# Kernel tuning notes

Hardware: AMD Instinct MI355X
Metric: run time of the kernel (lower is better)

Reference implementation:

```python
import jax, jax.numpy as jnp
import numpy as np

N, E, G = 8000, 32000, 256   # nodes, edges, graphs
F, H = 680, 10               # in-features, GAT heads
HF = F * H                   # 6800


def setup_inputs() -> dict:
    key = jax.random.key(0)
    ks = jax.random.split(key, 12)
    s = lambda i, shape, sc: (jax.random.normal(ks[i], shape, jnp.float32) * sc)
    x = jax.random.normal(ks[0], (N, F), jnp.float32)
    edge_index = jax.random.randint(ks[1], (2, E), 0, N)
    batch = jnp.arange(N) // (N // G)   # contiguous, every graph non-empty
    return dict(
        x=x, edge_index=edge_index, batch=batch,
        W_gat=s(2, (F, HF), 0.05), a_src=s(3, (H, F), 0.05), a_dst=s(4, (H, F), 0.05),
        b_gat=jnp.zeros((HF,), jnp.float32),
        W_gcn=s(5, (HF, HF), 0.01), b_gcn=jnp.zeros((HF,), jnp.float32),
        W1=s(6, (2 * HF, 512), 0.02), b1=jnp.zeros((512,), jnp.float32),
        W2=s(7, (512, 128), 0.05), b2=jnp.zeros((128,), jnp.float32),
        W3=s(8, (128, 64), 0.05), b3=jnp.zeros((64,), jnp.float32),
    )


def _self_loops(edge_index):
    loop = jnp.arange(N)
    return (jnp.concatenate([edge_index[0], loop]),
            jnp.concatenate([edge_index[1], loop]))


def _gat(x, src, dst, W, a_s, a_d, b):
    xh = (x @ W).reshape(N, H, F)                          # [N,H,F]
    al_s = jnp.einsum('nhf,hf->nh', xh, a_s)               # src attention logits
    al_d = jnp.einsum('nhf,hf->nh', xh, a_d)
    e = jax.nn.leaky_relu(al_s[src] + al_d[dst], 0.2)      # [Etot,H]
    m = jax.ops.segment_max(e, dst, num_segments=N)        # segment softmax over dst
    ex = jnp.exp(e - m[dst])
    z = jax.ops.segment_sum(ex, dst, num_segments=N)
    alpha = ex / (z[dst] + 1e-16)
    out = jax.ops.segment_sum(alpha[:, :, None] * xh[src], dst, num_segments=N)
    return out.reshape(N, HF) + b                          # concat heads + bias


def _gcn(x, src, dst, W, b):
    deg = jax.ops.segment_sum(jnp.ones_like(dst, jnp.float32), dst, num_segments=N)
    dinv = jax.lax.rsqrt(deg)                              # deg>=1 due to self-loops
    norm = dinv[src] * dinv[dst]
    xw = x @ W
    return jax.ops.segment_sum(norm[:, None] * xw[src], dst, num_segments=N) + b


def reference(x, edge_index, batch, W_gat, a_src, a_dst, b_gat, W_gcn, b_gcn,
              W1, b1, W2, b2, W3, b3):
    src, dst = _self_loops(edge_index)
    h = jax.nn.relu(_gat(x, src, dst, W_gat, a_src, a_dst, b_gat))  # dropout = id (eval)
    h = jax.nn.relu(_gcn(h, src, dst, W_gcn, b_gcn))
    gmp = jax.ops.segment_max(h, batch, num_segments=G)
    cnt = jax.ops.segment_sum(jnp.ones((N,), jnp.float32), batch, num_segments=G)
    gap = jax.ops.segment_sum(h, batch, num_segments=G) / cnt[:, None]
    g = jnp.concatenate([gmp, gap], axis=1)                # [G, 2*HF]
    g = jax.nn.relu(g @ W1 + b1)
    g = g @ W2 + b2
    return g @ W3 + b3                                     # [G, 64]
```

## Files before the change

kernel.cpp:

```cpp
#include <hip/hip_runtime.h>
#include <cstdint>
#include <cstddef>

#define DEVFN static __device__ __forceinline__

typedef __attribute__((ext_vector_type(8))) short short8;
typedef __attribute__((ext_vector_type(4))) float f32x4;

constexpr int NN  = 8000;
constexpr int NE  = 32000;
constexpr int ET  = NE + NN;
constexpr int NG  = 256;
constexpr int F   = 680;
constexpr int NH  = 10;
constexpr int HF  = 6800;

constexpr int MP   = 8192;
constexpr int KP1  = 704;
constexpr int NP   = 6912;
constexpr int KP2  = 6848;
constexpr int KM1P = 13632;

DEVFN unsigned short f2bf(float f) {
  unsigned u = __float_as_uint(f);
  u += 0x7fffu + ((u >> 16) & 1u);
  return (unsigned short)(u >> 16);
}
DEVFN float bf2f(unsigned short b) { return __uint_as_float(((unsigned)b) << 16); }

DEVFN int perm64(int k, int r) {
  return (((k >> 3) ^ (r & 7)) << 3) | (k & 7);
}

DEVFN void gload16(const void* g, void* l) {
  __builtin_amdgcn_global_load_lds(
      (const __attribute__((address_space(1))) unsigned int*)g,
      (__attribute__((address_space(3))) unsigned int*)l, 16, 0, 0);
}

DEVFN f32x4 mfma_16x16x32_bf16(short8 a, short8 b, f32x4 c) {
  asm("v_mfma_f32_16x16x32_bf16 %0, %1, %2, %0" : "+v"(c) : "v"(a), "v"(b));
  return c;
}

template<int OUT_MODE, bool BIAS, bool RELU, bool SWZ>
__global__ __launch_bounds__(512, 2) void gemm256(
    const unsigned short* __restrict__ A, const unsigned short* __restrict__ BT,
    void* __restrict__ C, const float* __restrict__ bias,
    int K, int cstride, int nvalid, int Mt, int KC) {
  __shared__ alignas(16) char Lds[131072];
  const int tid = threadIdx.x;
  const int wave = tid >> 6, lane = tid & 63;
  const int wm = wave >> 2, wn = wave & 3;
  const int g4 = lane >> 4, l15 = lane & 15;
  const int xorc = l15 & 7;
  const int brow = (wn & 1) * 64;

  int bm, bn;
  if (SWZ) {
    const int xcd = blockIdx.x & 7;
    const int j = blockIdx.x >> 3;
    bm = j & 31;
    bn = (j >> 5) * 8 + xcd;
    const int Nt = (nvalid + 255) >> 8;
    if (bn >= Nt) return;
  } else {
    bm = blockIdx.x % Mt;
    bn = blockIdx.x / Mt;
  }

  const int NTt = K >> 6;
  const int kb = blockIdx.z * KC;
  const int NT = min(KC, NTt - kb);
  const unsigned short* Ag = A + (size_t)bm * 256 * K + (size_t)kb * 64;
  const unsigned short* Bg = BT + (size_t)bn * 256 * K + (size_t)kb * 64;

  const int srow = tid >> 3;
  const int schk = (tid & 7) * 8;

  auto stageHalf = [&](const unsigned short* G, int t, int op, int h) {
    char* base = Lds + ((((t & 1) << 2) | (op << 1) | h) << 14) + (wave << 10);
    const unsigned short* src = G + (size_t)(h * 128 + srow) * K + (size_t)t * 64 + schk;
    gload16(src, base);
    gload16(src + (size_t)64 * K, base + 8192);
  };

  const char* Ab0 = Lds + (((0 << 2) | (0 << 1) | wm) << 14);
  const char* Ab1 = Lds + (((1 << 2) | (0 << 1) | wm) << 14);
  const char* Bb0 = Lds + (((0 << 2) | (1 << 1) | (wn >> 1)) << 14);
  const char* Bb1 = Lds + (((1 << 2) | (1 << 1) | (wn >> 1)) << 14);

  f32x4 acc[8][4];
#pragma unroll
  for (int i = 0; i < 8; i++)
#pragma unroll
    for (int j = 0; j < 4; j++) acc[i][j] = (f32x4){0.f, 0.f, 0.f, 0.f};

  short8 aR[4][2], b0[2][2], b1[2][2];

#define READ_A(BASE, QM) do {                                                   \
  _Pragma("unroll") for (int i2 = 0; i2 < 4; ++i2)                              \
  _Pragma("unroll") for (int ks = 0; ks < 2; ++ks)                              \
    aR[i2][ks] = *(const short8*)((BASE) + ((QM) * 64 + i2 * 16 + l15) * 128    \
                                  + ((((ks << 2) | g4) ^ xorc) << 4));          \
} while (0)

#define READ_B(BASE, QN, DST) do {                                              \
  _Pragma("unroll") for (int j2 = 0; j2 < 2; ++j2)                              \
  _Pragma("unroll") for (int ks = 0; ks < 2; ++ks)                              \
    DST[j2][ks] = *(const short8*)((BASE) + (brow + (QN) * 32 + j2 * 16 + l15) * 128 \
                                   + ((((ks << 2) | g4) ^ xorc) << 4));         \
} while (0)

#define MMAQ(QM, QN, BREG) do {                                                 \
  _Pragma("unroll") for (int i2 = 0; i2 < 4; ++i2)                              \
  _Pragma("unroll") for (int j2 = 0; j2 < 2; ++j2)                              \
  _Pragma("unroll") for (int ks = 0; ks < 2; ++ks)                              \
    acc[(QM) * 4 + i2][(QN) * 2 + j2] =                                         \
        mfma_16x16x32_bf16(aR[i2][ks], BREG[j2][ks], acc[(QM) * 4 + i2][(QN) * 2 + j2]); \
} while (0)

  if (NT > 0) {
    stageHalf(Ag, 0, 0, 0); stageHalf(Ag, 0, 0, 1);
    stageHalf(Bg, 0, 1, 0); stageHalf(Bg, 0, 1, 1);
  }
  if (NT > 1) {
    stageHalf(Ag, 1, 0, 0); stageHalf(Ag, 1, 0, 1);
    stageHalf(Bg, 1, 1, 0); stageHalf(Bg, 1, 1, 1);
    asm volatile("s_waitcnt vmcnt(8)" ::: "memory");
  } else {
    asm volatile("s_waitcnt vmcnt(0)" ::: "memory");
  }
  asm volatile("s_barrier" ::: "memory");

  for (int t = 0; t < NT; ++t) {
    const char* Ac = (t & 1) ? Ab1 : Ab0;
    const char* Bc = (t & 1) ? Bb1 : Bb0;
    const bool pf = (t + 2 < NT);

    READ_A(Ac, 0);
    READ_B(Bc, 0, b0);
    __builtin_amdgcn_s_setprio(1);
    MMAQ(0, 0, b0);
    __builtin_amdgcn_s_setprio(0);

    READ_B(Bc, 1, b1);
    __builtin_amdgcn_s_setprio(1);
    MMAQ(0, 1, b1);
    __builtin_amdgcn_s_setprio(0);

    asm volatile("s_barrier" ::: "memory");
    if (pf) { stageHalf(Bg, t + 2, 1, 0); stageHalf(Bg, t + 2, 1, 1); }

    READ_A(Ac, 1);
    __builtin_amdgcn_s_setprio(1);
    MMAQ(1, 1, b1);
    __builtin_amdgcn_s_setprio(0);

    asm volatile("s_barrier" ::: "memory");
    if (pf) { stageHalf(Ag, t + 2, 0, 0); stageHalf(Ag, t + 2, 0, 1); }

    __builtin_amdgcn_s_setprio(1);
    MMAQ(1, 0, b0);
    __builtin_amdgcn_s_setprio(0);

    if (pf) asm volatile("s_waitcnt vmcnt(8)" ::: "memory");
    else    asm volatile("s_waitcnt vmcnt(0)" ::: "memory");
    asm volatile("s_barrier" ::: "memory");
  }

#undef READ_A
#undef READ_B
#undef MMAQ

  const int m0 = bm * 256 + wm * 128;
  const int n0 = bn * 256 + wn * 64;
  const int rb = g4 * 4;
#pragma unroll
  for (int i = 0; i < 8; i++) {
#pragma unroll
    for (int j = 0; j < 4; j++) {
      int c = n0 + j * 16 + l15;
      if (c >= nvalid) continue;
      float bv = BIAS ? bias[c] : 0.f;
#pragma unroll
      for (int tt = 0; tt < 4; tt++) {
        int r = m0 + i * 16 + rb + tt;
        float v = acc[i][j][tt] + bv;
        if (RELU) v = fmaxf(v, 0.f);
        if (OUT_MODE == 0) {
          ((float*)C)[(size_t)r * cstride + c] = v;
        } else if (OUT_MODE == 1) {
          ((unsigned short*)C)[(size_t)r * cstride + c] = f2bf(v);
        } else if (OUT_MODE == 2) {
          int pos = (c & ~63) + perm64(c & 63, r);
          ((unsigned short*)C)[(size_t)r * cstride + pos] = f2bf(v);
        } else {
          ((float*)C)[(size_t)blockIdx.z * (Mt * 256) * cstride + (size_t)r * cstride + c] = v;
        }
      }
    }
  }
}

template<bool RELU>
__global__ void finish_kernel(const float* __restrict__ acc, const float* __restrict__ bias,
                              unsigned short* __restrict__ out, int S, int M, int N) {
  int idx = blockIdx.x * 256 + threadIdx.x;
  if (idx >= M * N) return;
  int r = idx / N, c = idx - r * N;
  float s = bias[c];
  for (int k = 0; k < S; k++) s += acc[(size_t)k * M * N + (size_t)r * N + c];
  if (RELU) s = fmaxf(s, 0.f);
  out[(size_t)r * N + (c & ~63) + perm64(c & 63, r)] = f2bf(s);
}

__global__ void conv_x_kernel(const float* __restrict__ x, unsigned short* __restrict__ out) {
  int idx = blockIdx.x * 256 + threadIdx.x;
  constexpr int GR = KP1 / 4;
  if (idx >= MP * GR) return;
  int row = idx / GR, k = (idx - row * GR) * 4;
  unsigned short v[4] = {0, 0, 0, 0};
  if (row < NN && k < F) {
    const float* p = x + (size_t)row * F + k;
    v[0] = f2bf(p[0]); v[1] = f2bf(p[1]); v[2] = f2bf(p[2]); v[3] = f2bf(p[3]);
  }
  int pos = (k & ~63) + perm64(k & 63, row);
  uint2 pk;
  pk.x = (unsigned)v[0] | ((unsigned)v[1] << 16);
  pk.y = (unsigned)v[2] | ((unsigned)v[3] << 16);
  *(uint2*)&out[(size_t)row * KP1 + pos] = pk;
}

__global__ void convT_kernel(const float* __restrict__ in, unsigned short* __restrict__ out,
                             int K, int N, int KPad, int NPad) {
  __shared__ float tile[32][33];
  int n0 = blockIdx.x * 32, k0 = blockIdx.y * 32;
  int tx = threadIdx.x, ty = threadIdx.y;
#pragma unroll
  for (int i = 0; i < 4; i++) {
    int k = k0 + ty + i * 8, n = n0 + tx;
    tile[ty + i * 8][tx] = (k < K && n < N) ? in[(size_t)k * N + n] : 0.f;
  }
  __syncthreads();
#pragma unroll
  for (int i = 0; i < 4; i++) {
    int n = n0 + ty + i * 8, k = k0 + tx;
    if (n < NPad && k < KPad) {
      int pos = (k & ~63) + perm64(k & 63, n);
      out[(size_t)n * KPad + pos] = f2bf(tile[tx][ty + i * 8]);
    }
  }
}

__global__ void logits_kernel(const unsigned short* __restrict__ xh,
                              const float* __restrict__ a_src, const float* __restrict__ a_dst,
                              float* __restrict__ al_s, float* __restrict__ al_d) {
  int wid = blockIdx.x * 4 + (threadIdx.x >> 6);
  int lane = threadIdx.x & 63;
  int n = wid / NH, h = wid - n * NH;
  if (n >= NN) return;
  const unsigned short* row = xh + (size_t)n * NP + h * F;
  const float* as = a_src + h * F;
  const float* ad = a_dst + h * F;
  float ss = 0.f, sd = 0.f;
  for (int f0 = lane; f0 < F; f0 += 64) {
    float v = bf2f(row[f0]);
    ss += v * as[f0]; sd += v * ad[f0];
  }
#pragma unroll
  for (int o = 32; o > 0; o >>= 1) { ss += __shfl_down(ss, o); sd += __shfl_down(sd, o); }
  if (lane == 0) { al_s[wid] = ss; al_d[wid] = sd; }
}

__global__ void edge_count_kernel(const int* __restrict__ ei, int* __restrict__ deg) {
  int e = blockIdx.x * 256 + threadIdx.x;
  if (e >= ET) return;
  int d = (e < NE) ? ei[NE + e] : (e - NE);
  atomicAdd(&deg[d], 1);
}

__global__ void scan_kernel(const int* __restrict__ deg, int* __restrict__ rs,
                            int* __restrict__ cursor) {
  __shared__ int part[1024];
  int t = threadIdx.x;
  int base = t * 8, s = 0, loc[8];
#pragma unroll
  for (int i = 0; i < 8; i++) { loc[i] = s; int idx = base + i; s += (idx < NN) ? deg[idx] : 0; }
  part[t] = s;
  __syncthreads();
  for (int off = 1; off < 1024; off <<= 1) {
    int v = (t >= off) ? part[t - off] : 0;
    __syncthreads();
    part[t] += v;
    __syncthreads();
  }
  int pre = (t > 0) ? part[t - 1] : 0;
#pragma unroll
  for (int i = 0; i < 8; i++) {
    int idx = base + i;
    if (idx <= NN) { rs[idx] = pre + loc[i]; cursor[idx] = pre + loc[i]; }
  }
}

__global__ void edge_fill_kernel(const int* __restrict__ ei, int* __restrict__ cursor,
                                 int* __restrict__ eidx) {
  int e = blockIdx.x * 256 + threadIdx.x;
  if (e >= ET) return;
  int d = (e < NE) ? ei[NE + e] : (e - NE);
  int pos = atomicAdd(&cursor[d], 1);
  eidx[pos] = e;
}

__global__ void dinv_kernel(const int* __restrict__ deg, float* __restrict__ dinv) {
  int n = blockIdx.x * 256 + threadIdx.x;
  if (n < NN) dinv[n] = rsqrtf((float)max(deg[n], 1));
}

__global__ void alpha_kernel(const int* __restrict__ ei, const int* __restrict__ rs,
                             const int* __restrict__ eidx, const float* __restrict__ al_s,
                             const float* __restrict__ al_d, float* __restrict__ alpha) {
  int w = blockIdx.x * 256 + threadIdx.x;
  if (w >= NN * NH) return;
  int n = w / NH, h = w - n * NH;
  int s0 = rs[n], s1 = rs[n + 1];
  float ad = al_d[w];
  float m = -3.0e38f;
  for (int i = s0; i < s1; i++) {
    int e = eidx[i]; int s = (e < NE) ? ei[e] : (e - NE);
    float x = al_s[s * NH + h] + ad;
    x = (x > 0.f) ? x : 0.2f * x;
    m = fmaxf(m, x);
  }
  float z = 0.f;
  for (int i = s0; i < s1; i++) {
    int e = eidx[i]; int s = (e < NE) ? ei[e] : (e - NE);
    float x = al_s[s * NH + h] + ad;
    x = (x > 0.f) ? x : 0.2f * x;
    float ex = __expf(x - m);
    alpha[(size_t)i * NH + h] = ex;
    z += ex;
  }
  float inv = 1.f / (z + 1e-16f);
  for (int i = s0; i < s1; i++) alpha[(size_t)i * NH + h] *= inv;
}

__global__ void gat_agg_kernel(const unsigned short* __restrict__ xh, const int* __restrict__ ei,
                               const int* __restrict__ rs, const int* __restrict__ eidx,
                               const float* __restrict__ alpha, const float* __restrict__ bgat,
                               unsigned short* __restrict__ hbf) {
  int n = blockIdx.x, t = threadIdx.x;
  int s0 = rs[n], s1 = rs[n + 1];
  for (int c4 = t; c4 < KP2 / 4; c4 += 256) {
    int c = c4 * 4;
    int pos = (c & ~63) + perm64(c & 63, n);
    if (c >= HF) {
      *(uint2*)&hbf[(size_t)n * KP2 + pos] = make_uint2(0u, 0u);
      continue;
    }
    int h = c / F;
    float a0 = 0.f, a1 = 0.f, a2 = 0.f, a3 = 0.f;
    for (int i = s0; i < s1; i++) {
      int e = eidx[i]; int s = (e < NE) ? ei[e] : (e - NE);
      float al = alpha[(size_t)i * NH + h];
      uint2 r = *(const uint2*)&xh[(size_t)s * NP + c];
      a0 += al * bf2f((unsigned short)(r.x & 0xffff));
      a1 += al * bf2f((unsigned short)(r.x >> 16));
      a2 += al * bf2f((unsigned short)(r.y & 0xffff));
      a3 += al * bf2f((unsigned short)(r.y >> 16));
    }
    a0 = fmaxf(a0 + bgat[c], 0.f);     a1 = fmaxf(a1 + bgat[c + 1], 0.f);
    a2 = fmaxf(a2 + bgat[c + 2], 0.f); a3 = fmaxf(a3 + bgat[c + 3], 0.f);
    uint2 pk;
    pk.x = (unsigned)f2bf(a0) | ((unsigned)f2bf(a1) << 16);
    pk.y = (unsigned)f2bf(a2) | ((unsigned)f2bf(a3) << 16);
    *(uint2*)&hbf[(size_t)n * KP2 + pos] = pk;
  }
}

__global__ void gcn_agg_kernel(const unsigned short* __restrict__ xw, const int* __restrict__ ei,
                               const int* __restrict__ rs, const int* __restrict__ eidx,
                               const float* __restrict__ dinv, const float* __restrict__ bgcn,
                               unsigned short* __restrict__ h2) {
  int n = blockIdx.x, t = threadIdx.x;
  int s0 = rs[n], s1 = rs[n + 1];
  float dn = dinv[n];
  for (int c4 = t; c4 < HF / 4; c4 += 256) {
    int c = c4 * 4;
    float a0 = 0.f, a1 = 0.f, a2 = 0.f, a3 = 0.f;
    for (int i = s0; i < s1; i++) {
      int e = eidx[i]; int s = (e < NE) ? ei[e] : (e - NE);
      float w = dinv[s] * dn;
      uint2 r = *(const uint2*)&xw[(size_t)s * NP + c];
      a0 += w * bf2f((unsigned short)(r.x & 0xffff));
      a1 += w * bf2f((unsigned short)(r.x >> 16));
      a2 += w * bf2f((unsigned short)(r.y & 0xffff));
      a3 += w * bf2f((unsigned short)(r.y >> 16));
    }
    a0 = fmaxf(a0 + bgcn[c], 0.f);     a1 = fmaxf(a1 + bgcn[c + 1], 0.f);
    a2 = fmaxf(a2 + bgcn[c + 2], 0.f); a3 = fmaxf(a3 + bgcn[c + 3], 0.f);
    uint2 pk;
    pk.x = (unsigned)f2bf(a0) | ((unsigned)f2bf(a1) << 16);
    pk.y = (unsigned)f2bf(a2) | ((unsigned)f2bf(a3) << 16);
    *(uint2*)&h2[(size_t)n * KP2 + c] = pk;
  }
}

__global__ void pool_init_kernel(int* gstart, int* gend, int* gcnt) {
  int g = threadIdx.x;
  gstart[g] = 0x7fffffff; gend[g] = 0; gcnt[g] = 0;
}
__global__ void pool_scan_kernel(const int* __restrict__ batch, int* gstart, int* gend, int* gcnt) {
  int n = blockIdx.x * 256 + threadIdx.x;
  if (n >= NN) return;
  int b = batch[n];
  if (b >= 0 && b < NG) {
    atomicMin(&gstart[b], n);
    atomicMax(&gend[b], n + 1);
    atomicAdd(&gcnt[b], 1);
  }
}
__global__ void pool_kernel(const unsigned short* __restrict__ h2, const int* __restrict__ batch,
                            const int* __restrict__ gstart, const int* __restrict__ gend,
                            const int* __restrict__ gcnt, unsigned short* __restrict__ gbf) {
  int g = blockIdx.x, t = threadIdx.x;
  int s = gstart[g], e = gend[g];
  float cnt = (float)max(gcnt[g], 1);
  for (int c = t; c < HF; c += 256) {
    float vmax = -3.0e38f, vsum = 0.f;
    for (int n = s; n < e; n++) {
      if (batch[n] != g) continue;
      float v = bf2f(h2[(size_t)n * KP2 + c]);
      vmax = fmaxf(vmax, v);
      vsum += v;
    }
    int c1 = c, c2 = HF + c;
    gbf[(size_t)g * KM1P + (c1 & ~63) + perm64(c1 & 63, g)] = f2bf(vmax);
    gbf[(size_t)g * KM1P + (c2 & ~63) + perm64(c2 & 63, g)] = f2bf(vsum / cnt);
  }
}

extern "C" void kernel_launch(void* const* d_in, const int* in_sizes, int n_in,
                              void* d_out, int out_size, void* d_ws, size_t ws_size,
                              hipStream_t stream) {
  (void)in_sizes; (void)n_in; (void)out_size; (void)ws_size;
  const float* x     = (const float*)d_in[0];
  const int*   ei    = (const int*)d_in[1];
  const int*   batch = (const int*)d_in[2];
  const float* W_gat = (const float*)d_in[3];
  const float* a_src = (const float*)d_in[4];
  const float* a_dst = (const float*)d_in[5];
  const float* b_gat = (const float*)d_in[6];
  const float* W_gcn = (const float*)d_in[7];
  const float* b_gcn = (const float*)d_in[8];
  const float* W1    = (const float*)d_in[9];
  const float* b1    = (const float*)d_in[10];
  const float* W2    = (const float*)d_in[11];
  const float* b2    = (const float*)d_in[12];
  const float* W3    = (const float*)d_in[13];
  const float* b3    = (const float*)d_in[14];
  float* out = (float*)d_out;

  char* ws = (char*)d_ws;
  size_t off = 0;
  auto alloc = [&](size_t bytes) -> void* {
    void* p = ws + off;
    off += (bytes + 255) & ~(size_t)255;
    return p;
  };
  unsigned short* bufA  = (unsigned short*)alloc((size_t)MP * NP * 2);
  unsigned short* bufB  = (unsigned short*)alloc((size_t)MP * KP2 * 2);
  unsigned short* wgcnT = (unsigned short*)alloc((size_t)NP * KP2 * 2);
  unsigned short* xbf   = (unsigned short*)alloc((size_t)MP * KP1 * 2);
  unsigned short* wgatT = (unsigned short*)alloc((size_t)NP * KP1 * 2);
  unsigned short* w1T   = (unsigned short*)alloc((size_t)512 * KM1P * 2);
  unsigned short* gbf   = (unsigned short*)alloc((size_t)NG * KM1P * 2);
  unsigned short* w2T   = (unsigned short*)alloc((size_t)256 * 512 * 2);
  unsigned short* w3T   = (unsigned short*)alloc((size_t)256 * 128 * 2);
  unsigned short* g1bf  = (unsigned short*)alloc((size_t)NG * 512 * 2);
  unsigned short* g2bf  = (unsigned short*)alloc((size_t)NG * 128 * 2);
  float* accf  = (float*)alloc((size_t)8 * 256 * 512 * 4);
  float* al_s  = (float*)alloc((size_t)NN * NH * 4);
  float* al_d  = (float*)alloc((size_t)NN * NH * 4);
  float* alpha = (float*)alloc((size_t)ET * NH * 4);
  float* dinv  = (float*)alloc((size_t)NN * 4);
  int* deg    = (int*)alloc((size_t)NN * 4);
  int* rs     = (int*)alloc((size_t)(NN + 1) * 4);
  int* cursor = (int*)alloc((size_t)(NN + 1) * 4);
  int* eidx   = (int*)alloc((size_t)ET * 4);
  int* gstart = (int*)alloc((size_t)NG * 4);
  int* gend   = (int*)alloc((size_t)NG * 4);
  int* gcnt   = (int*)alloc((size_t)NG * 4);

  constexpr int MT = MP / 256;
  constexpr int GRID_SWZ = 32 * 32;

  conv_x_kernel<<<(MP * (KP1 / 4)) / 256, 256, 0, stream>>>(x, xbf);
  convT_kernel<<<dim3(NP / 32, KP1 / 32), dim3(32, 8), 0, stream>>>(W_gat, wgatT, F, HF, KP1, NP);
  convT_kernel<<<dim3(NP / 32, KP2 / 32), dim3(32, 8), 0, stream>>>(W_gcn, wgcnT, HF, HF, KP2, NP);
  convT_kernel<<<dim3(512 / 32, KM1P / 32), dim3(32, 8), 0, stream>>>(W1, w1T, 2 * HF, 512, KM1P, 512);
  convT_kernel<<<dim3(256 / 32, 512 / 32), dim3(32, 8), 0, stream>>>(W2, w2T, 512, 128, 512, 256);
  convT_kernel<<<dim3(256 / 32, 128 / 32), dim3(32, 8), 0, stream>>>(W3, w3T, 128, 64, 128, 256);
  hipMemsetAsync(deg, 0, (size_t)NN * 4, stream);
  hipMemsetAsync((char*)bufB + (size_t)NN * KP2 * 2, 0, (size_t)(MP - NN) * KP2 * 2, stream);
  hipMemsetAsync(gbf, 0, (size_t)NG * KM1P * 2, stream);

  gemm256<1, false, false, true><<<dim3(GRID_SWZ, 1, 1), 512, 0, stream>>>(
      xbf, wgatT, bufA, nullptr, KP1, NP, NP, MT, KP1 / 64);

  logits_kernel<<<(NN * NH) / 4, 256, 0, stream>>>(bufA, a_src, a_dst, al_s, al_d);

  edge_count_kernel<<<(ET + 255) / 256, 256, 0, stream>>>(ei, deg);
  scan_kernel<<<1, 1024, 0, stream>>>(deg, rs, cursor);
  edge_fill_kernel<<<(ET + 255) / 256, 256, 0, stream>>>(ei, cursor, eidx);
  dinv_kernel<<<(NN + 255) / 256, 256, 0, stream>>>(deg, dinv);

  alpha_kernel<<<(NN * NH + 255) / 256, 256, 0, stream>>>(ei, rs, eidx, al_s, al_d, alpha);

  gat_agg_kernel<<<NN, 256, 0, stream>>>(bufA, ei, rs, eidx, alpha, b_gat, bufB);

  gemm256<1, false, false, true><<<dim3(GRID_SWZ, 1, 1), 512, 0, stream>>>(
      bufB, wgcnT, bufA, nullptr, KP2, NP, NP, MT, KP2 / 64);

  gcn_agg_kernel<<<NN, 256, 0, stream>>>(bufA, ei, rs, eidx, dinv, b_gcn, bufB);

  pool_init_kernel<<<1, 256, 0, stream>>>(gstart, gend, gcnt);
  pool_scan_kernel<<<(NN + 255) / 256, 256, 0, stream>>>(batch, gstart, gend, gcnt);
  pool_kernel<<<NG, 256, 0, stream>>>(bufB, batch, gstart, gend, gcnt, gbf);

  gemm256<3, false, false, false><<<dim3(1 * 2, 1, 8), 512, 0, stream>>>(
      gbf, w1T, accf, nullptr, KM1P, 512, 512, 1, 27);
  finish_kernel<true><<<(256 * 512) / 256, 256, 0, stream>>>(accf, b1, g1bf, 8, 256, 512);

  gemm256<3, false, false, false><<<dim3(1, 1, 4), 512, 0, stream>>>(
      g1bf, w2T, accf, nullptr, 512, 128, 128, 1, 2);
  finish_kernel<false><<<(256 * 128) / 256, 256, 0, stream>>>(accf, b2, g2bf, 4, 256, 128);

  gemm256<0, true, false, false><<<dim3(1, 1, 1), 512, 0, stream>>>(
      g2bf, w3T, out, b3, 128, 64, 64, 1, 2);
}
```

Baseline: 1.623 ms.

## Switch GEMM to 32x32 MFMA with register prefetch; vectorize aggregation and pooling

The GEMM core moves from 16x16x32 to 32x32x16 bf16 MFMA with double-buffered register fragments, and the main loop is reorganized to issue a single tile-wide stage per iteration. The GAT and GCN aggregation kernels now cache neighbor indices and weights in shared memory and use 8-wide bf16 loads. The pooling kernel drops the per-node batch check, which assumes contiguous graph membership, and uses vectorized loads and stores. These changes target MFMA issue overhead, LDS read count and memory-access width, at the cost of higher register pressure in the GEMM.

```diff
diff --git a/kernel.cpp b/kernel.cpp
--- a/kernel.cpp
+++ b/kernel.cpp
@@ -5,7 +5,7 @@
 #define DEVFN static __device__ __forceinline__
 
 typedef __attribute__((ext_vector_type(8))) short short8;
-typedef __attribute__((ext_vector_type(4))) float f32x4;
+typedef __attribute__((ext_vector_type(16))) float f32x16;
 
 constexpr int NN  = 8000;
 constexpr int NE  = 32000;
@@ -38,8 +38,8 @@
       (__attribute__((address_space(3))) unsigned int*)l, 16, 0, 0);
 }
 
-DEVFN f32x4 mfma_16x16x32_bf16(short8 a, short8 b, f32x4 c) {
-  asm("v_mfma_f32_16x16x32_bf16 %0, %1, %2, %0" : "+v"(c) : "v"(a), "v"(b));
+DEVFN f32x16 mfma32(short8 a, short8 b, f32x16 c) {
+  asm("v_mfma_f32_32x32x16_bf16 %0, %1, %2, %0" : "+v"(c) : "v"(a), "v"(b));
   return c;
 }
 
@@ -52,8 +52,7 @@
   const int tid = threadIdx.x;
   const int wave = tid >> 6, lane = tid & 63;
   const int wm = wave >> 2, wn = wave & 3;
-  const int g4 = lane >> 4, l15 = lane & 15;
-  const int xorc = l15 & 7;
+  const int l31 = lane & 31, hi = lane >> 5, l7 = lane & 7;
   const int brow = (wn & 1) * 64;
 
   int bm, bn;
@@ -84,109 +83,101 @@
     gload16(src, base);
     gload16(src + (size_t)64 * K, base + 8192);
   };
+  auto stageTile = [&](int t) {
+    stageHalf(Ag, t, 0, 0); stageHalf(Ag, t, 0, 1);
+    stageHalf(Bg, t, 1, 0); stageHalf(Bg, t, 1, 1);
+  };
 
   const char* Ab0 = Lds + (((0 << 2) | (0 << 1) | wm) << 14);
   const char* Ab1 = Lds + (((1 << 2) | (0 << 1) | wm) << 14);
   const char* Bb0 = Lds + (((0 << 2) | (1 << 1) | (wn >> 1)) << 14);
   const char* Bb1 = Lds + (((1 << 2) | (1 << 1) | (wn >> 1)) << 14);
 
-  f32x4 acc[8][4];
-#pragma unroll
-  for (int i = 0; i < 8; i++)
-#pragma unroll
-    for (int j = 0; j < 4; j++) acc[i][j] = (f32x4){0.f, 0.f, 0.f, 0.f};
-
-  short8 aR[4][2], b0[2][2], b1[2][2];
-
-#define READ_A(BASE, QM) do {                                                   \
-  _Pragma("unroll") for (int i2 = 0; i2 < 4; ++i2)                              \
-  _Pragma("unroll") for (int ks = 0; ks < 2; ++ks)                              \
-    aR[i2][ks] = *(const short8*)((BASE) + ((QM) * 64 + i2 * 16 + l15) * 128    \
-                                  + ((((ks << 2) | g4) ^ xorc) << 4));          \
+  const int aoff = l31 * 128;
+  const int boff = (brow + l31) * 128;
+
+  f32x16 acc[4][2];
+#pragma unroll
+  for (int i = 0; i < 4; i++)
+#pragma unroll
+    for (int j = 0; j < 2; j++) acc[i][j] = (f32x16)(0.f);
+
+  short8 a0[4], a1[4], b0v[2], b1v[2];
+
+#define RD_A(DST, ABASE, KS) do {                                               \
+  _Pragma("unroll") for (int m = 0; m < 4; ++m)                                 \
+    DST[m] = *(const short8*)((ABASE) + m * 4096 + aoff                         \
+                              + (((2 * (KS) + hi) ^ l7) << 4));                 \
 } while (0)
 
-#define READ_B(BASE, QN, DST) do {                                              \
-  _Pragma("unroll") for (int j2 = 0; j2 < 2; ++j2)                              \
-  _Pragma("unroll") for (int ks = 0; ks < 2; ++ks)                              \
-    DST[j2][ks] = *(const short8*)((BASE) + (brow + (QN) * 32 + j2 * 16 + l15) * 128 \
-                                   + ((((ks << 2) | g4) ^ xorc) << 4));         \
+#define RD_B(DST, BBASE, KS) do {                                               \
+  _Pragma("unroll") for (int n = 0; n < 2; ++n)                                 \
+    DST[n] = *(const short8*)((BBASE) + n * 4096 + boff                         \
+                              + (((2 * (KS) + hi) ^ l7) << 4));                 \
 } while (0)
 
-#define MMAQ(QM, QN, BREG) do {                                                 \
-  _Pragma("unroll") for (int i2 = 0; i2 < 4; ++i2)                              \
-  _Pragma("unroll") for (int j2 = 0; j2 < 2; ++j2)                              \
-  _Pragma("unroll") for (int ks = 0; ks < 2; ++ks)                              \
-    acc[(QM) * 4 + i2][(QN) * 2 + j2] =                                         \
-        mfma_16x16x32_bf16(aR[i2][ks], BREG[j2][ks], acc[(QM) * 4 + i2][(QN) * 2 + j2]); \
+#define MM(ASET, BSET) do {                                                     \
+  __builtin_amdgcn_s_setprio(1);                                                \
+  _Pragma("unroll") for (int m = 0; m < 4; ++m)                                 \
+  _Pragma("unroll") for (int n = 0; n < 2; ++n)                                 \
+    acc[m][n] = mfma32(ASET[m], BSET[n], acc[m][n]);                            \
+  __builtin_amdgcn_s_setprio(0);                                                \
 } while (0)
 
-  if (NT > 0) {
-    stageHalf(Ag, 0, 0, 0); stageHalf(Ag, 0, 0, 1);
-    stageHalf(Bg, 0, 1, 0); stageHalf(Bg, 0, 1, 1);
-  }
   if (NT > 1) {
-    stageHalf(Ag, 1, 0, 0); stageHalf(Ag, 1, 0, 1);
-    stageHalf(Bg, 1, 1, 0); stageHalf(Bg, 1, 1, 1);
+    stageTile(0); stageTile(1);
     asm volatile("s_waitcnt vmcnt(8)" ::: "memory");
   } else {
+    stageTile(0);
     asm volatile("s_waitcnt vmcnt(0)" ::: "memory");
   }
   asm volatile("s_barrier" ::: "memory");
+  RD_A(a0, Ab0, 0); RD_B(b0v, Bb0, 0);
 
   for (int t = 0; t < NT; ++t) {
     const char* Ac = (t & 1) ? Ab1 : Ab0;
     const char* Bc = (t & 1) ? Bb1 : Bb0;
-    const bool pf = (t + 2 < NT);
-
-    READ_A(Ac, 0);
-    READ_B(Bc, 0, b0);
-    __builtin_amdgcn_s_setprio(1);
-    MMAQ(0, 0, b0);
-    __builtin_amdgcn_s_setprio(0);
-
-    READ_B(Bc, 1, b1);
-    __builtin_amdgcn_s_setprio(1);
-    MMAQ(0, 1, b1);
-    __builtin_amdgcn_s_setprio(0);
-
+    const char* An = (t & 1) ? Ab0 : Ab1;
+    const char* Bn = (t & 1) ? Bb0 : Bb1;
+
+    RD_A(a1, Ac, 1); RD_B(b1v, Bc, 1);
+    MM(a0, b0v);
+    RD_A(a0, Ac, 2); RD_B(b0v, Bc, 2);
+    MM(a1, b1v);
+    RD_A(a1, Ac, 3); RD_B(b1v, Bc, 3);
+    MM(a0, b0v);
+    asm volatile("s_waitcnt lgkmcnt(0)" ::: "memory");
     asm volatile("s_barrier" ::: "memory");
-    if (pf) { stageHalf(Bg, t + 2, 1, 0); stageHalf(Bg, t + 2, 1, 1); }
-
-    READ_A(Ac, 1);
-    __builtin_amdgcn_s_setprio(1);
-    MMAQ(1, 1, b1);
-    __builtin_amdgcn_s_setprio(0);
-
-    asm volatile("s_barrier" ::: "memory");
-    if (pf) { stageHalf(Ag, t + 2, 0, 0); stageHalf(Ag, t + 2, 0, 1); }
-
-    __builtin_amdgcn_s_setprio(1);
-    MMAQ(1, 0, b0);
-    __builtin_amdgcn_s_setprio(0);
-
-    if (pf) asm volatile("s_waitcnt vmcnt(8)" ::: "memory");
-    else    asm volatile("s_waitcnt vmcnt(0)" ::: "memory");
-    asm volatile("s_barrier" ::: "memory");
-  }
-
-#undef READ_A
-#undef READ_B
-#undef MMAQ
+    if (t + 2 < NT) {
+      stageTile(t + 2);
+      asm volatile("s_waitcnt vmcnt(8)" ::: "memory");
+    } else if (t + 1 < NT) {
+      asm volatile("s_waitcnt vmcnt(0)" ::: "memory");
+    }
+    if (t + 1 < NT) {
+      asm volatile("s_barrier" ::: "memory");
+      RD_A(a0, An, 0); RD_B(b0v, Bn, 0);
+    }
+    MM(a1, b1v);
+  }
+
+#undef RD_A
+#undef RD_B
+#undef MM
 
   const int m0 = bm * 256 + wm * 128;
   const int n0 = bn * 256 + wn * 64;
-  const int rb = g4 * 4;
-#pragma unroll
-  for (int i = 0; i < 8; i++) {
-#pragma unroll
-    for (int j = 0; j < 4; j++) {
-      int c = n0 + j * 16 + l15;
+#pragma unroll
+  for (int mf = 0; mf < 4; ++mf) {
+#pragma unroll
+    for (int nf = 0; nf < 2; ++nf) {
+      int c = n0 + nf * 32 + l31;
       if (c >= nvalid) continue;
       float bv = BIAS ? bias[c] : 0.f;
 #pragma unroll
-      for (int tt = 0; tt < 4; tt++) {
-        int r = m0 + i * 16 + rb + tt;
-        float v = acc[i][j][tt] + bv;
+      for (int reg = 0; reg < 16; ++reg) {
+        int r = m0 + mf * 32 + (reg & 3) + 8 * (reg >> 2) + 4 * hi;
+        float v = acc[mf][nf][reg] + bv;
         if (RELU) v = fmaxf(v, 0.f);
         if (OUT_MODE == 0) {
           ((float*)C)[(size_t)r * cstride + c] = v;
@@ -345,64 +336,92 @@
   for (int i = s0; i < s1; i++) alpha[(size_t)i * NH + h] *= inv;
 }
 
-__global__ void gat_agg_kernel(const unsigned short* __restrict__ xh, const int* __restrict__ ei,
-                               const int* __restrict__ rs, const int* __restrict__ eidx,
-                               const float* __restrict__ alpha, const float* __restrict__ bgat,
-                               unsigned short* __restrict__ hbf) {
+DEVFN void axpy8(float al, uint4 r, float* a) {
+  a[0] += al * bf2f((unsigned short)(r.x & 0xffff));
+  a[1] += al * bf2f((unsigned short)(r.x >> 16));
+  a[2] += al * bf2f((unsigned short)(r.y & 0xffff));
+  a[3] += al * bf2f((unsigned short)(r.y >> 16));
+  a[4] += al * bf2f((unsigned short)(r.z & 0xffff));
+  a[5] += al * bf2f((unsigned short)(r.z >> 16));
+  a[6] += al * bf2f((unsigned short)(r.w & 0xffff));
+  a[7] += al * bf2f((unsigned short)(r.w >> 16));
+}
+DEVFN uint4 pack8(const float* a) {
+  uint4 p;
+  p.x = (unsigned)f2bf(a[0]) | ((unsigned)f2bf(a[1]) << 16);
+  p.y = (unsigned)f2bf(a[2]) | ((unsigned)f2bf(a[3]) << 16);
+  p.z = (unsigned)f2bf(a[4]) | ((unsigned)f2bf(a[5]) << 16);
+  p.w = (unsigned)f2bf(a[6]) | ((unsigned)f2bf(a[7]) << 16);
+  return p;
+}
+
+constexpr int MAXE = 256;
+
+__global__ __launch_bounds__(256) void gat_agg_kernel(
+    const unsigned short* __restrict__ xh, const int* __restrict__ ei,
+    const int* __restrict__ rs, const int* __restrict__ eidx,
+    const float* __restrict__ alpha, const float* __restrict__ bgat,
+    unsigned short* __restrict__ hbf) {
+  __shared__ int   Ls[MAXE];
+  __shared__ float La[MAXE][NH];
   int n = blockIdx.x, t = threadIdx.x;
-  int s0 = rs[n], s1 = rs[n + 1];
-  for (int c4 = t; c4 < KP2 / 4; c4 += 256) {
-    int c = c4 * 4;
-    int pos = (c & ~63) + perm64(c & 63, n);
+  int s0 = rs[n], d = rs[n + 1] - s0;
+  int dc = min(d, MAXE);
+  for (int i = t; i < dc; i += 256) {
+    int e = eidx[s0 + i]; Ls[i] = (e < NE) ? ei[e] : (e - NE);
+  }
+  for (int j = t; j < dc * NH; j += 256)
+    La[j / NH][j % NH] = alpha[(size_t)(s0 + j / NH) * NH + j % NH];
+  __syncthreads();
+  for (int c8 = t; c8 < KP2 / 8; c8 += 256) {
+    int c = c8 * 8;
+    int pos = (c & ~63) + ((((c >> 3) & 7) ^ (n & 7)) << 3);
     if (c >= HF) {
-      *(uint2*)&hbf[(size_t)n * KP2 + pos] = make_uint2(0u, 0u);
+      *(uint4*)&hbf[(size_t)n * KP2 + pos] = make_uint4(0u, 0u, 0u, 0u);
       continue;
     }
     int h = c / F;
-    float a0 = 0.f, a1 = 0.f, a2 = 0.f, a3 = 0.f;
-    for (int i = s0; i < s1; i++) {
-      int e = eidx[i]; int s = (e < NE) ? ei[e] : (e - NE);
-      float al = alpha[(size_t)i * NH + h];
-      uint2 r = *(const uint2*)&xh[(size_t)s * NP + c];
-      a0 += al * bf2f((unsigned short)(r.x & 0xffff));
-      a1 += al * bf2f((unsigned short)(r.x >> 16));
-      a2 += al * bf2f((unsigned short)(r.y & 0xffff));
-      a3 += al * bf2f((unsigned short)(r.y >> 16));
-    }
-    a0 = fmaxf(a0 + bgat[c], 0.f);     a1 = fmaxf(a1 + bgat[c + 1], 0.f);
-    a2 = fmaxf(a2 + bgat[c + 2], 0.f); a3 = fmaxf(a3 + bgat[c + 3], 0.f);
-    uint2 pk;
-    pk.x = (unsigned)f2bf(a0) | ((unsigned)f2bf(a1) << 16);
-    pk.y = (unsigned)f2bf(a2) | ((unsigned)f2bf(a3) << 16);
-    *(uint2*)&hbf[(size_t)n * KP2 + pos] = pk;
-  }
-}
-
-__global__ void gcn_agg_kernel(const unsigned short* __restrict__ xw, const int* __restrict__ ei,
-                               const int* __restrict__ rs, const int* __restrict__ eidx,
-                               const float* __restrict__ dinv, const float* __restrict__ bgcn,
-                               unsigned short* __restrict__ h2) {
+    float a[8] = {0.f, 0.f, 0.f, 0.f, 0.f, 0.f, 0.f, 0.f};
+    for (int i = 0; i < dc; ++i)
+      axpy8(La[i][h], *(const uint4*)&xh[(size_t)Ls[i] * NP + c], a);
+    for (int i = MAXE; i < d; ++i) {
+      int e = eidx[s0 + i]; int s = (e < NE) ? ei[e] : (e - NE);
+      axpy8(alpha[(size_t)(s0 + i) * NH + h], *(const uint4*)&xh[(size_t)s * NP + c], a);
+    }
+#pragma unroll
+    for (int q = 0; q < 8; ++q) a[q] = fmaxf(a[q] + bgat[c + q], 0.f);
+    *(uint4*)&hbf[(size_t)n * KP2 + pos] = pack8(a);
+  }
+}
+
+__global__ __launch_bounds__(256) void gcn_agg_kernel(
+    const unsigned short* __restrict__ xw, const int* __restrict__ ei,
+    const int* __restrict__ rs, const int* __restrict__ eidx,
+    const float* __restrict__ dinv, const float* __restrict__ bgcn,
+    unsigned short* __restrict__ h2) {
+  __shared__ int   Ls[MAXE];
+  __shared__ float Lw[MAXE];
   int n = blockIdx.x, t = threadIdx.x;
-  int s0 = rs[n], s1 = rs[n + 1];
+  int s0 = rs[n], d = rs[n + 1] - s0;
+  int dc = min(d, MAXE);
   float dn = dinv[n];
-  for (int c4 = t; c4 < HF / 4; c4 += 256) {
-    int c = c4 * 4;
-    float a0 = 0.f, a1 = 0.f, a2 = 0.f, a3 = 0.f;
-    for (int i = s0; i < s1; i++) {
-      int e = eidx[i]; int s = (e < NE) ? ei[e] : (e - NE);
-      float w = dinv[s] * dn;
-      uint2 r = *(const uint2*)&xw[(size_t)s * NP + c];
-      a0 += w * bf2f((unsigned short)(r.x & 0xffff));
-      a1 += w * bf2f((unsigned short)(r.x >> 16));
-      a2 += w * bf2f((unsigned short)(r.y & 0xffff));
-      a3 += w * bf2f((unsigned short)(r.y >> 16));
-    }
-    a0 = fmaxf(a0 + bgcn[c], 0.f);     a1 = fmaxf(a1 + bgcn[c + 1], 0.f);
-    a2 = fmaxf(a2 + bgcn[c + 2], 0.f); a3 = fmaxf(a3 + bgcn[c + 3], 0.f);
-    uint2 pk;
-    pk.x = (unsigned)f2bf(a0) | ((unsigned)f2bf(a1) << 16);
-    pk.y = (unsigned)f2bf(a2) | ((unsigned)f2bf(a3) << 16);
-    *(uint2*)&h2[(size_t)n * KP2 + c] = pk;
+  for (int i = t; i < dc; i += 256) {
+    int e = eidx[s0 + i]; int s = (e < NE) ? ei[e] : (e - NE);
+    Ls[i] = s; Lw[i] = dinv[s] * dn;
+  }
+  __syncthreads();
+  for (int c8 = t; c8 < HF / 8; c8 += 256) {
+    int c = c8 * 8;
+    float a[8] = {0.f, 0.f, 0.f, 0.f, 0.f, 0.f, 0.f, 0.f};
+    for (int i = 0; i < dc; ++i)
+      axpy8(Lw[i], *(const uint4*)&xw[(size_t)Ls[i] * NP + c], a);
+    for (int i = MAXE; i < d; ++i) {
+      int e = eidx[s0 + i]; int s = (e < NE) ? ei[e] : (e - NE);
+      axpy8(dinv[s] * dn, *(const uint4*)&xw[(size_t)s * NP + c], a);
+    }
+#pragma unroll
+    for (int q = 0; q < 8; ++q) a[q] = fmaxf(a[q] + bgcn[c + q], 0.f);
+    *(uint4*)&h2[(size_t)n * KP2 + c] = pack8(a);
   }
 }
 
@@ -420,23 +439,34 @@
     atomicAdd(&gcnt[b], 1);
   }
 }
-__global__ void pool_kernel(const unsigned short* __restrict__ h2, const int* __restrict__ batch,
+__global__ void pool_kernel(const unsigned short* __restrict__ h2,
                             const int* __restrict__ gstart, const int* __restrict__ gend,
                             const int* __restrict__ gcnt, unsigned short* __restrict__ gbf) {
   int g = blockIdx.x, t = threadIdx.x;
   int s = gstart[g], e = gend[g];
-  float cnt = (float)max(gcnt[g], 1);
-  for (int c = t; c < HF; c += 256) {
-    float vmax = -3.0e38f, vsum = 0.f;
-    for (int n = s; n < e; n++) {
-      if (batch[n] != g) continue;
-      float v = bf2f(h2[(size_t)n * KP2 + c]);
-      vmax = fmaxf(vmax, v);
-      vsum += v;
-    }
-    int c1 = c, c2 = HF + c;
-    gbf[(size_t)g * KM1P + (c1 & ~63) + perm64(c1 & 63, g)] = f2bf(vmax);
-    gbf[(size_t)g * KM1P + (c2 & ~63) + perm64(c2 & 63, g)] = f2bf(vsum / cnt);
+  float inv = 1.f / (float)max(gcnt[g], 1);
+  for (int c8 = t; c8 < HF / 8; c8 += 256) {
+    int c = c8 * 8;
+    float mx[8], sm[8];
+#pragma unroll
+    for (int q = 0; q < 8; ++q) { mx[q] = -3.0e38f; sm[q] = 0.f; }
+    for (int n = s; n < e; ++n) {
+      uint4 r = *(const uint4*)&h2[(size_t)n * KP2 + c];
+      float v[8];
+      v[0] = bf2f((unsigned short)(r.x & 0xffff)); v[1] = bf2f((unsigned short)(r.x >> 16));
+      v[2] = bf2f((unsigned short)(r.y & 0xffff)); v[3] = bf2f((unsigned short)(r.y >> 16));
+      v[4] = bf2f((unsigned short)(r.z & 0xffff)); v[5] = bf2f((unsigned short)(r.z >> 16));
+      v[6] = bf2f((unsigned short)(r.w & 0xffff)); v[7] = bf2f((unsigned short)(r.w >> 16));
+#pragma unroll
+      for (int q = 0; q < 8; ++q) { mx[q] = fmaxf(mx[q], v[q]); sm[q] += v[q]; }
+    }
+#pragma unroll
+    for (int q = 0; q < 8; ++q) sm[q] *= inv;
+    int c2 = HF + c;
+    int pos1 = (c & ~63) + ((((c >> 3) & 7) ^ (g & 7)) << 3);
+    int pos2 = (c2 & ~63) + ((((c2 >> 3) & 7) ^ (g & 7)) << 3);
+    *(uint4*)&gbf[(size_t)g * KM1P + pos1] = pack8(mx);
+    *(uint4*)&gbf[(size_t)g * KM1P + pos2] = pack8(sm);
   }
 }
 
@@ -526,7 +556,7 @@
 
   pool_init_kernel<<<1, 256, 0, stream>>>(gstart, gend, gcnt);
   pool_scan_kernel<<<(NN + 255) / 256, 256, 0, stream>>>(batch, gstart, gend, gcnt);
-  pool_kernel<<<NG, 256, 0, stream>>>(bufB, batch, gstart, gend, gcnt, gbf);
+  pool_kernel<<<NG, 256, 0, stream>>>(bufB, gstart, gend, gcnt, gbf);
 
   gemm256<3, false, false, false><<<dim3(1 * 2, 1, 8), 512, 0, stream>>>(
       gbf, w1T, accf, nullptr, KM1P, 512, 512, 1, 27);
```

Measured after the change: 1.422 ms. 1.14x faster.
